# Kernel tuning notes

Hardware: AMD Instinct MI355X
Metric: run time of the kernel (lower is better)

Reference implementation:

```python
import jax, jax.numpy as jnp
import numpy as np

N_HEAD, D_HEAD, D_MODEL = 16, 64, 1024
BSZ, QLEN, MEMLEN = 4, 1024, 1024
KLEN = QLEN + MEMLEN
LN_EPS = 1e-5


def _rel_shift(x):
    # x: [b, q, k, n] -> Transformer-XL relative shift
    b, q, k, n = x.shape
    x = jnp.pad(x, ((0, 0), (0, 0), (1, 0), (0, 0)))  # [b, q, k+1, n]
    x = x.reshape(b, k + 1, q, n)[:, 1:]
    return x.reshape(b, q, k, n)


def _layer_norm(x, gamma, beta):
    mu = jnp.mean(x, axis=-1, keepdims=True)
    var = jnp.var(x, axis=-1, keepdims=True)
    return (x - mu) * jax.lax.rsqrt(var + LN_EPS) * gamma + beta


def setup_inputs() -> dict:
    key = jax.random.key(0)
    ks = jax.random.split(key, 8)
    w = jax.random.normal(ks[0], (BSZ, QLEN, D_MODEL), dtype=jnp.float32)
    r = jax.random.normal(ks[1], (1, KLEN, D_MODEL), dtype=jnp.float32)
    mem = jax.random.normal(ks[2], (BSZ, MEMLEN, D_MODEL), dtype=jnp.float32)
    # causal mask: key j visible iff j <= i + MEMLEN; 1 = masked
    i = jnp.arange(QLEN)[:, None]
    j = jnp.arange(KLEN)[None, :]
    attention_mask = (j > i + MEMLEN).astype(jnp.int32)
    s = 0.02
    qkv_w = jax.random.normal(ks[3], (3 * N_HEAD * D_HEAD, D_MODEL), dtype=jnp.float32) * s
    r_w = jax.random.normal(ks[4], (N_HEAD * D_HEAD, D_MODEL), dtype=jnp.float32) * s
    o_w = jax.random.normal(ks[5], (D_MODEL, N_HEAD * D_HEAD), dtype=jnp.float32) * s
    r_r_bias = jax.random.normal(ks[6], (N_HEAD, D_HEAD), dtype=jnp.float32) * s
    r_w_bias = jax.random.normal(ks[7], (N_HEAD, D_HEAD), dtype=jnp.float32) * s
    ln_gamma = jnp.ones((D_MODEL,), dtype=jnp.float32)
    ln_beta = jnp.zeros((D_MODEL,), dtype=jnp.float32)
    return {"w": w, "r": r, "mem": mem, "attention_mask": attention_mask,
            "qkv_w": qkv_w, "r_w": r_w, "o_w": o_w,
            "r_r_bias": r_r_bias, "r_w_bias": r_w_bias,
            "ln_gamma": ln_gamma, "ln_beta": ln_beta}


def reference(w, r, mem, attention_mask, qkv_w, r_w, o_w, r_r_bias, r_w_bias, ln_gamma, ln_beta):
    bsz, qlen, d_model = w.shape
    n_head, d_head = r_r_bias.shape
    scale = 1.0 / (d_head ** 0.5)
    cat = jnp.concatenate([mem, w], axis=1)                 # [b, klen, dm]
    heads = cat @ qkv_w.T                                   # post-lnorm: no pre-LN
    q, k, v = jnp.split(heads, 3, axis=-1)
    q = q[:, -qlen:]
    klen = k.shape[1]
    q = q.reshape(bsz, qlen, n_head, d_head)
    k = k.reshape(bsz, klen, n_head, d_head)
    v = v.reshape(bsz, klen, n_head, d_head)
    rk = (r @ r_w.T).reshape(-1, n_head, d_head)            # [rlen, n, d]
    AC = jnp.einsum('bind,bjnd->bijn', q + r_w_bias, k)
    BD = _rel_shift(jnp.einsum('bind,jnd->bijn', q + r_r_bias, rk))
    score = (AC + BD) * scale                               # [b, q, k, n]
    mask = (attention_mask == 1)[None, :, :, None]
    score = jnp.where(mask, -1e30, score)
    prob = jax.nn.softmax(score, axis=2)                    # softmax over keys
    vec = jnp.einsum('bijn,bjnd->bind', prob, v).reshape(bsz, qlen, n_head * d_head)
    attn_out = vec @ o_w.T
    # post layer-norm, deepnorm_alpha defaults to 1.0, dropout is identity (eval)
    return _layer_norm(w + attn_out, ln_gamma, ln_beta)
```

## Files before the change

kernel.cpp:

```cpp
#include <hip/hip_runtime.h>

typedef __attribute__((ext_vector_type(8))) __bf16 bf16x8;
typedef __attribute__((ext_vector_type(4))) __bf16 bf16x4;
typedef __attribute__((ext_vector_type(4))) float f32x4;

__device__ __forceinline__ f32x4 mfma16(bf16x8 a, bf16x8 b, f32x4 c) {
  return __builtin_amdgcn_mfma_f32_16x16x32_bf16(a, b, c, 0, 0, 0);
}

__device__ __forceinline__ void gload_lds16(const void* g, void* l) {
  __builtin_amdgcn_global_load_lds(
      (__attribute__((address_space(1))) void*)(void*)g,
      (__attribute__((address_space(3))) void*)l, 16, 0, 0);
}

__device__ __forceinline__ bf16x8 ldsfrag(const __bf16* base, int row, int lc) {
  return *(const bf16x8*)(base + row * 64 + ((lc ^ (row & 7)) << 3));
}


__global__ __launch_bounds__(256) void cast_plain(const float* __restrict__ in,
                                                  __bf16* __restrict__ out) {
  size_t t = (size_t)blockIdx.x * 256 + threadIdx.x;
  const float4* p = (const float4*)(in + t * 8);
  float4 a = p[0], b = p[1];
  bf16x8 v;
  v[0] = (__bf16)a.x; v[1] = (__bf16)a.y; v[2] = (__bf16)a.z; v[3] = (__bf16)a.w;
  v[4] = (__bf16)b.x; v[5] = (__bf16)b.y; v[6] = (__bf16)b.z; v[7] = (__bf16)b.w;
  *(bf16x8*)(out + t * 8) = v;
}

__global__ __launch_bounds__(256) void cast_cat(const float* __restrict__ mem,
                                                const float* __restrict__ w,
                                                __bf16* __restrict__ out) {
  size_t t = (size_t)blockIdx.x * 256 + threadIdx.x;
  size_t o = t * 8;
  int c = (int)(o & 1023);
  int row = (int)(o >> 10);
  int tt = row & 2047;
  int b = row >> 11;
  const float* src = (tt < 1024)
      ? (mem + ((size_t)(b * 1024 + tt) * 1024 + c))
      : (w + ((size_t)(b * 1024 + (tt - 1024)) * 1024 + c));
  float4 a = ((const float4*)src)[0], d = ((const float4*)src)[1];
  bf16x8 v;
  v[0] = (__bf16)a.x; v[1] = (__bf16)a.y; v[2] = (__bf16)a.z; v[3] = (__bf16)a.w;
  v[4] = (__bf16)d.x; v[5] = (__bf16)d.y; v[6] = (__bf16)d.z; v[7] = (__bf16)d.w;
  *(bf16x8*)(out + o) = v;
}

template <int MODE>
__global__ __launch_bounds__(256, 2) void gemm_bt(const __bf16* __restrict__ A,
                                                  const __bf16* __restrict__ B,
                                                  __bf16* __restrict__ Cb,
                                                  float* __restrict__ Cf,
                                                  const float* __restrict__ Res,
                                                  int M, int N, int K) {
  __shared__ __bf16 As[128 * 32];
  __shared__ __bf16 Bs[128 * 32];
  const int tid = threadIdx.x;
  const int wid = tid >> 6, lane = tid & 63;
  const int l15 = lane & 15, lhi = lane >> 4;
  const int wr = wid >> 1, wc = wid & 1;
  const size_t arow0 = (size_t)blockIdx.y * 128;
  const size_t brow0 = (size_t)blockIdx.x * 128;

  f32x4 acc[4][4] = {};

  const int c0 = tid, c1 = tid + 256;
  const int r0 = c0 >> 2, o0 = (c0 & 3) * 8;
  const int r1 = c1 >> 2, o1 = (c1 & 3) * 8;
  const __bf16* ga0 = A + (arow0 + r0) * K + o0;
  const __bf16* ga1 = A + (arow0 + r1) * K + o1;
  const __bf16* gb0 = B + (brow0 + r0) * K + o0;
  const __bf16* gb1 = B + (brow0 + r1) * K + o1;
  __bf16* la0 = As + wid * 512;
  __bf16* la1 = As + 2048 + wid * 512;
  __bf16* lb0 = Bs + wid * 512;
  __bf16* lb1 = Bs + 2048 + wid * 512;

  for (int k0 = 0; k0 < K; k0 += 32) {
    gload_lds16(ga0 + k0, la0);
    gload_lds16(ga1 + k0, la1);
    gload_lds16(gb0 + k0, lb0);
    gload_lds16(gb1 + k0, lb1);
    __syncthreads();
    bf16x8 af[4], bf[4];
#pragma unroll
    for (int m = 0; m < 4; ++m)
      af[m] = *(const bf16x8*)(As + (wr * 64 + m * 16 + l15) * 32 + lhi * 8);
#pragma unroll
    for (int n = 0; n < 4; ++n)
      bf[n] = *(const bf16x8*)(Bs + (wc * 64 + n * 16 + l15) * 32 + lhi * 8);
#pragma unroll
    for (int m = 0; m < 4; ++m)
#pragma unroll
      for (int n = 0; n < 4; ++n)
        acc[m][n] = mfma16(af[m], bf[n], acc[m][n]);
    __syncthreads();
  }

#pragma unroll
  for (int m = 0; m < 4; ++m)
#pragma unroll
    for (int n = 0; n < 4; ++n) {
      size_t row = arow0 + wr * 64 + m * 16 + lhi * 4;
      size_t col = brow0 + wc * 64 + n * 16 + l15;
#pragma unroll
      for (int j = 0; j < 4; ++j) {
        size_t idx = (row + j) * (size_t)N + col;
        float v = acc[m][n][j];
        if (MODE == 0) Cb[idx] = (__bf16)v;
        else Cf[idx] = v + Res[idx];
      }
    }
}

__global__ __launch_bounds__(256) void vtrans_kernel(const __bf16* __restrict__ heads,
                                                     __bf16* __restrict__ vT) {
  __shared__ __bf16 T[64][66];
  const int j0 = blockIdx.x * 64;
  const int h = blockIdx.y, b = blockIdx.z;
  const int tid = threadIdx.x;
  {
    int jj = tid >> 2, dq = tid & 3;
    const __bf16* src = heads + ((size_t)(b * 2048 + j0 + jj)) * 3072 + 2048 + h * 64 + dq * 16;
    bf16x8 a = *(const bf16x8*)src;
    bf16x8 c = *(const bf16x8*)(src + 8);
#pragma unroll
    for (int e = 0; e < 8; ++e) { T[jj][dq * 16 + e] = a[e]; T[jj][dq * 16 + 8 + e] = c[e]; }
  }
  __syncthreads();
  {
    int d = tid >> 2, jq = tid & 3;
    bf16x8 o0, o1;
#pragma unroll
    for (int e = 0; e < 8; ++e) { o0[e] = T[jq * 16 + e][d]; o1[e] = T[jq * 16 + 8 + e][d]; }
    __bf16* dst = vT + ((size_t)((b * 16 + h) * 64 + d)) * 2048 + j0 + jq * 16;
    *(bf16x8*)dst = o0;
    *(bf16x8*)(dst + 8) = o1;
  }
}

__global__ __launch_bounds__(256) void ackb_kernel(const __bf16* __restrict__ heads,
                                                   const float* __restrict__ r_w_bias,
                                                   float* __restrict__ ackb) {
  int gid = blockIdx.x * 256 + threadIdx.x;
  int j = gid & 2047, bh = gid >> 11, b = bh >> 4, h = bh & 15;
  const __bf16* kp = heads + ((size_t)(b * 2048 + j)) * 3072 + 1024 + h * 64;
  const float* bw = r_w_bias + h * 64;
  float s = 0.f;
#pragma unroll
  for (int o = 0; o < 8; ++o) {
    bf16x8 kv = *(const bf16x8*)(kp + o * 8);
#pragma unroll
    for (int e = 0; e < 8; ++e) s += (float)kv[e] * bw[o * 8 + e];
  }
  ackb[(size_t)bh * 2048 + j] = s * 0.125f;
}

__global__ __launch_bounds__(256) void brk_kernel(const __bf16* __restrict__ rk,
                                                  const float* __restrict__ r_r_bias,
                                                  float* __restrict__ brk) {
  int gid = blockIdx.x * 256 + threadIdx.x;
  int t = gid % 2304, h = gid / 2304;
  float s = 0.f;
  if (t < 2048) {
    const __bf16* rp = rk + (size_t)t * 1024 + h * 64;
    const float* br = r_r_bias + h * 64;
#pragma unroll
    for (int o = 0; o < 8; ++o) {
      bf16x8 rv = *(const bf16x8*)(rp + o * 8);
#pragma unroll
      for (int e = 0; e < 8; ++e) s += (float)rv[e] * br[o * 8 + e];
    }
  }
  brk[(size_t)h * 2304 + t] = s * 0.125f;
}

__global__ __launch_bounds__(256, 3) void attn_kernel(
    const __bf16* __restrict__ heads, const __bf16* __restrict__ rk,
    const __bf16* __restrict__ vT, const float* __restrict__ ackb,
    const float* __restrict__ brk, __bf16* __restrict__ vec) {
  __shared__ __bf16 Ks[64 * 64];
  __shared__ __bf16 Vt[64 * 64];
  __shared__ __bf16 Ring[128 * 64];
  __shared__ __bf16 BPa[4][16 * 88];

  const int lin = blockIdx.x;
  const int seq = lin >> 3;
  const int bq = 15 - (seq >> 3);
  const int rem = seq & 7;
  const int b = rem >> 1;
  const int h = (lin & 7) + ((rem & 1) << 3);
  const int base = bq << 6;

  const int tid = threadIdx.x;
  const int wid = tid >> 6, lane = tid & 63;
  const int l15 = lane & 15, lhi = lane >> 4;
  const int i0 = base + wid * 16;

  const int srow8 = lane >> 3;
  const int sch = (lane & 7) ^ (srow8 & 7);

  bf16x8 q0, q1;
  {
    const __bf16* qp =
        heads + ((size_t)(b * 2048 + 1024 + i0 + l15)) * 3072 + h * 64 + lhi * 8;
    bf16x8 a = *(const bf16x8*)qp;
    bf16x8 c = *(const bf16x8*)(qp + 32);
#pragma unroll
    for (int e = 0; e < 8; ++e) {
      q0[e] = (__bf16)((float)a[e] * 0.125f);
      q1[e] = (__bf16)((float)c[e] * 0.125f);
    }
  }

  const float* ackbp = ackb + ((size_t)(b * 16 + h)) * 2048;
  const float* brkp = brk + (size_t)h * 2304;
  __bf16* BP = BPa[wid];

  float m_run = -1e30f, l_run = 0.f;
  f32x4 accv[4] = {};

  {
    int r0 = 960 - base + wid * 16 + srow8;
    gload_lds16(rk + (size_t)r0 * 1024 + h * 64 + sch * 8,
                Ring + (((960 - base) + wid * 16) & 127) * 64);
    gload_lds16(rk + (size_t)(r0 + 8) * 1024 + h * 64 + sch * 8,
                Ring + (((960 - base) + wid * 16 + 8) & 127) * 64);
  }

  const int jmaxb = min(2048, base + 1088);
  for (int j0 = 0; j0 < jmaxb; j0 += 64) {
    __syncthreads();
    {
      const __bf16* kst =
          heads + ((size_t)(b * 2048 + j0 + wid * 16 + srow8)) * 3072 + 1024 + h * 64 + sch * 8;
      gload_lds16(kst, Ks + wid * 16 * 64);
      gload_lds16(kst + (size_t)8 * 3072, Ks + (wid * 16 + 8) * 64);
      const __bf16* vst =
          vT + ((size_t)((b * 16 + h) * 64 + wid * 16 + srow8)) * 2048 + j0 + sch * 8;
      gload_lds16(vst, Vt + wid * 16 * 64);
      gload_lds16(vst + (size_t)8 * 2048, Vt + (wid * 16 + 8) * 64);
      int T0 = j0 + 1024 - base;
      int rr = T0 + wid * 16 + srow8;
      gload_lds16(rk + (size_t)min(rr, 2047) * 1024 + h * 64 + sch * 8,
                  Ring + ((T0 + wid * 16) & 127) * 64);
      gload_lds16(rk + (size_t)min(rr + 8, 2047) * 1024 + h * 64 + sch * 8,
                  Ring + ((T0 + wid * 16 + 8) & 127) * 64);
    }
    __syncthreads();
    if (j0 >= i0 + 1040) continue;

    const int tbase = j0 + 1008 - i0;

#pragma unroll
    for (int ct = 0; ct < 5; ++ct) {
      int slot = (tbase + ct * 16 + l15) & 127;
      bf16x8 a0 = ldsfrag(Ring, slot, lhi);
      bf16x8 a1 = ldsfrag(Ring, slot, 4 + lhi);
      f32x4 init = *(const f32x4*)(brkp + tbase + ct * 16 + lhi * 4);
      f32x4 bd = mfma16(a1, q1, mfma16(a0, q0, init));
      bf16x4 bv;
      bv[0] = (__bf16)bd[0]; bv[1] = (__bf16)bd[1];
      bv[2] = (__bf16)bd[2]; bv[3] = (__bf16)bd[3];
      *(bf16x4*)(BP + l15 * 88 + ct * 16 + lhi * 4) = bv;
    }

    f32x4 st[4];
#pragma unroll
    for (int jt = 0; jt < 4; ++jt) {
      bf16x8 k0 = ldsfrag(Ks, jt * 16 + l15, lhi);
      bf16x8 k1 = ldsfrag(Ks, jt * 16 + l15, 4 + lhi);
      f32x4 init = *(const f32x4*)(ackbp + j0 + jt * 16 + lhi * 4);
      st[jt] = mfma16(k1, q1, mfma16(k0, q0, init));
    }

    float sv[4][4];
#pragma unroll
    for (int jt = 0; jt < 4; ++jt)
#pragma unroll
      for (int r2 = 0; r2 < 4; ++r2) {
        int jl = jt * 16 + lhi * 4 + r2;
        float v = st[jt][r2] + (float)BP[l15 * 88 + jl + 15 - l15];
        bool msk = (j0 + jl) > (i0 + l15 + 1024);
        sv[jt][r2] = msk ? -1e30f : v;
      }

    float mx = sv[0][0];
#pragma unroll
    for (int jt = 0; jt < 4; ++jt)
#pragma unroll
      for (int r2 = 0; r2 < 4; ++r2) mx = fmaxf(mx, sv[jt][r2]);
    mx = fmaxf(mx, __shfl_xor(mx, 16, 64));
    mx = fmaxf(mx, __shfl_xor(mx, 32, 64));
    float mn = fmaxf(m_run, mx);
    float corr = __expf(m_run - mn);
    float rs = 0.f;
#pragma unroll
    for (int jt = 0; jt < 4; ++jt)
#pragma unroll
      for (int r2 = 0; r2 < 4; ++r2) {
        float p = __expf(sv[jt][r2] - mn);
        sv[jt][r2] = p;
        rs += p;
      }
    rs += __shfl_xor(rs, 16, 64);
    rs += __shfl_xor(rs, 32, 64);
    m_run = mn;
    l_run = l_run * corr + rs;

    float c4[4];
#pragma unroll
    for (int r2 = 0; r2 < 4; ++r2) c4[r2] = __shfl(corr, lhi * 4 + r2, 64);
#pragma unroll
    for (int dt = 0; dt < 4; ++dt)
#pragma unroll
      for (int r2 = 0; r2 < 4; ++r2) accv[dt][r2] *= c4[r2];

#pragma unroll
    for (int jt = 0; jt < 4; ++jt) {
      bf16x4 pv;
      pv[0] = (__bf16)sv[jt][0]; pv[1] = (__bf16)sv[jt][1];
      pv[2] = (__bf16)sv[jt][2]; pv[3] = (__bf16)sv[jt][3];
      *(bf16x4*)(BP + l15 * 88 + jt * 16 + lhi * 4) = pv;
    }
    bf16x8 ap0 = *(const bf16x8*)(BP + l15 * 88 + lhi * 8);
    bf16x8 ap1 = *(const bf16x8*)(BP + l15 * 88 + 32 + lhi * 8);
#pragma unroll
    for (int dt = 0; dt < 4; ++dt) {
      bf16x8 vf0 = ldsfrag(Vt, dt * 16 + l15, lhi);
      bf16x8 vf1 = ldsfrag(Vt, dt * 16 + l15, 4 + lhi);
      accv[dt] = mfma16(ap1, vf1, mfma16(ap0, vf0, accv[dt]));
    }
  }

  float inv4[4];
#pragma unroll
  for (int r2 = 0; r2 < 4; ++r2) inv4[r2] = 1.0f / __shfl(l_run, lhi * 4 + r2, 64);
#pragma unroll
  for (int dt = 0; dt < 4; ++dt)
#pragma unroll
    for (int r2 = 0; r2 < 4; ++r2) {
      int i = i0 + lhi * 4 + r2;
      float v = accv[dt][r2] * inv4[r2];
      vec[((size_t)(b * 1024 + i)) * 1024 + h * 64 + dt * 16 + l15] = (__bf16)v;
    }
}

__global__ __launch_bounds__(256) void ln_kernel(const float* __restrict__ pre,
                                                 const float* __restrict__ gamma,
                                                 const float* __restrict__ beta,
                                                 float* __restrict__ out) {
  const int row = blockIdx.x;
  const int tid = threadIdx.x;
  const float4 v = ((const float4*)(pre + (size_t)row * 1024))[tid];
  float s = v.x + v.y + v.z + v.w;
  float s2 = v.x * v.x + v.y * v.y + v.z * v.z + v.w * v.w;
#pragma unroll
  for (int off = 1; off < 64; off <<= 1) {
    s += __shfl_xor(s, off, 64);
    s2 += __shfl_xor(s2, off, 64);
  }
  __shared__ float red[8];
  const int wid = tid >> 6;
  if ((tid & 63) == 0) { red[wid * 2] = s; red[wid * 2 + 1] = s2; }
  __syncthreads();
  s = red[0] + red[2] + red[4] + red[6];
  s2 = red[1] + red[3] + red[5] + red[7];
  float mu = s * (1.0f / 1024.0f);
  float var = s2 * (1.0f / 1024.0f) - mu * mu;
  float rstd = rsqrtf(var + 1e-5f);
  float4 g = ((const float4*)gamma)[tid];
  float4 be = ((const float4*)beta)[tid];
  float4 o;
  o.x = (v.x - mu) * rstd * g.x + be.x;
  o.y = (v.y - mu) * rstd * g.y + be.y;
  o.z = (v.z - mu) * rstd * g.z + be.z;
  o.w = (v.w - mu) * rstd * g.w + be.w;
  ((float4*)(out + (size_t)row * 1024))[tid] = o;
}

extern "C" void kernel_launch(void* const* d_in, const int* in_sizes, int n_in,
                              void* d_out, int out_size, void* d_ws, size_t ws_size,
                              hipStream_t stream) {
  const float* w = (const float*)d_in[0];
  const float* r = (const float*)d_in[1];
  const float* mem = (const float*)d_in[2];
  const float* qkv_w = (const float*)d_in[4];
  const float* r_w = (const float*)d_in[5];
  const float* o_w = (const float*)d_in[6];
  const float* r_r_bias = (const float*)d_in[7];
  const float* r_w_bias = (const float*)d_in[8];
  const float* gamma = (const float*)d_in[9];
  const float* beta = (const float*)d_in[10];
  float* out = (float*)d_out;

  char* ws = (char*)d_ws;
  const size_t MB = 1024 * 1024;
  __bf16* catB = (__bf16*)(ws + 0);
  __bf16* vT = (__bf16*)(ws + 0);
  float* pre = (float*)(ws + 0);
  __bf16* qkvwB = (__bf16*)(ws + 16 * MB);
  __bf16* rB = (__bf16*)(ws + 22 * MB);
  __bf16* rwB = (__bf16*)(ws + 26 * MB);
  __bf16* owB = (__bf16*)(ws + 28 * MB);
  __bf16* headsB = (__bf16*)(ws + 30 * MB);
  __bf16* rkB = (__bf16*)(ws + 78 * MB);
  __bf16* vecB = (__bf16*)(ws + 82 * MB);
  float* ackbF = (float*)(ws + 90 * MB);
  float* brkF = (float*)(ws + 91 * MB);

  cast_cat<<<4096, 256, 0, stream>>>(mem, w, catB);
  cast_plain<<<1536, 256, 0, stream>>>(qkv_w, qkvwB);
  cast_plain<<<1024, 256, 0, stream>>>(r, rB);
  cast_plain<<<512, 256, 0, stream>>>(r_w, rwB);
  cast_plain<<<512, 256, 0, stream>>>(o_w, owB);

  gemm_bt<0><<<dim3(24, 64), 256, 0, stream>>>(catB, qkvwB, headsB, nullptr, nullptr,
                                               8192, 3072, 1024);
  gemm_bt<0><<<dim3(8, 16), 256, 0, stream>>>(rB, rwB, rkB, nullptr, nullptr,
                                              2048, 1024, 1024);

  vtrans_kernel<<<dim3(32, 16, 4), 256, 0, stream>>>(headsB, vT);
  ackb_kernel<<<512, 256, 0, stream>>>(headsB, r_w_bias, ackbF);
  brk_kernel<<<144, 256, 0, stream>>>(rkB, r_r_bias, brkF);

  attn_kernel<<<1024, 256, 0, stream>>>(headsB, rkB, vT, ackbF, brkF, vecB);

  gemm_bt<1><<<dim3(8, 32), 256, 0, stream>>>(vecB, owB, nullptr, pre, w,
                                              4096, 1024, 1024);
  ln_kernel<<<4096, 256, 0, stream>>>(pre, gamma, beta, out);
}
```

Measured before the change: 298.3 us.

## Double-buffer attention K/V, register-prefetch rk, lazy rescale, skip unused Q GEMM tiles

The attention kernel now double-buffers the K and V tiles in LDS and drops the second barrier per iteration. The rk fragments are prefetched straight into registers in place of the LDS ring buffer. Softmax switches to exp2 with log2e folded into the scale, masking is confined to diagonal tiles, and the running-max rescale of the accumulator only happens when the max grows by more than a threshold. The QKV GEMM also skips the tiles that compute Q for memory rows, which are never used. The changes trade more LDS per block (and the dropped occupancy hint) for less waiting on loads and barriers. The lazy rescale lets values exceed 1 before normalisation, which can reduce accuracy.

```diff
diff --git a/kernel.cpp b/kernel.cpp
--- a/kernel.cpp
+++ b/kernel.cpp
@@ -3,6 +3,8 @@
 typedef __attribute__((ext_vector_type(8))) __bf16 bf16x8;
 typedef __attribute__((ext_vector_type(4))) __bf16 bf16x4;
 typedef __attribute__((ext_vector_type(4))) float f32x4;
+
+#define SCALE_LOG2E 0.18033688011112042f
 
 __device__ __forceinline__ f32x4 mfma16(bf16x8 a, bf16x8 b, f32x4 c) {
   return __builtin_amdgcn_mfma_f32_16x16x32_bf16(a, b, c, 0, 0, 0);
@@ -55,7 +57,8 @@
                                                   __bf16* __restrict__ Cb,
                                                   float* __restrict__ Cf,
                                                   const float* __restrict__ Res,
-                                                  int M, int N, int K) {
+                                                  int M, int N, int K, int skipq) {
+  if (skipq && blockIdx.x < 8 && (blockIdx.y & 15) < 8) return;
   __shared__ __bf16 As[128 * 32];
   __shared__ __bf16 Bs[128 * 32];
   const int tid = threadIdx.x;
@@ -156,7 +159,7 @@
 #pragma unroll
     for (int e = 0; e < 8; ++e) s += (float)kv[e] * bw[o * 8 + e];
   }
-  ackb[(size_t)bh * 2048 + j] = s * 0.125f;
+  ackb[(size_t)bh * 2048 + j] = s * SCALE_LOG2E;
 }
 
 __global__ __launch_bounds__(256) void brk_kernel(const __bf16* __restrict__ rk,
@@ -175,17 +178,16 @@
       for (int e = 0; e < 8; ++e) s += (float)rv[e] * br[o * 8 + e];
     }
   }
-  brk[(size_t)h * 2304 + t] = s * 0.125f;
-}
-
-__global__ __launch_bounds__(256, 3) void attn_kernel(
+  brk[(size_t)h * 2304 + t] = s * SCALE_LOG2E;
+}
+
+__global__ __launch_bounds__(256) void attn_kernel(
     const __bf16* __restrict__ heads, const __bf16* __restrict__ rk,
     const __bf16* __restrict__ vT, const float* __restrict__ ackb,
     const float* __restrict__ brk, __bf16* __restrict__ vec) {
-  __shared__ __bf16 Ks[64 * 64];
-  __shared__ __bf16 Vt[64 * 64];
-  __shared__ __bf16 Ring[128 * 64];
-  __shared__ __bf16 BPa[4][16 * 88];
+  __shared__ __bf16 Ks[2 * 4096];
+  __shared__ __bf16 Vt[2 * 4096];
+  __shared__ __bf16 Pool[4][2112];
 
   const int lin = blockIdx.x;
   const int seq = lin >> 3;
@@ -211,68 +213,79 @@
     bf16x8 c = *(const bf16x8*)(qp + 32);
 #pragma unroll
     for (int e = 0; e < 8; ++e) {
-      q0[e] = (__bf16)((float)a[e] * 0.125f);
-      q1[e] = (__bf16)((float)c[e] * 0.125f);
+      q0[e] = (__bf16)((float)a[e] * SCALE_LOG2E);
+      q1[e] = (__bf16)((float)c[e] * SCALE_LOG2E);
     }
   }
 
   const float* ackbp = ackb + ((size_t)(b * 16 + h)) * 2048;
   const float* brkp = brk + (size_t)h * 2304;
-  __bf16* BP = BPa[wid];
+  __bf16* BPW = Pool[wid];
 
   float m_run = -1e30f, l_run = 0.f;
   f32x4 accv[4] = {};
 
+#define STAGE_KV(J0, BUF)                                                              \
+  do {                                                                                 \
+    const __bf16* kst = heads +                                                        \
+        ((size_t)(b * 2048 + (J0) + wid * 16 + srow8)) * 3072 + 1024 + h * 64 + sch * 8; \
+    gload_lds16(kst, Ks + (BUF) * 4096 + wid * 16 * 64);                               \
+    gload_lds16(kst + (size_t)8 * 3072, Ks + (BUF) * 4096 + (wid * 16 + 8) * 64);      \
+    const __bf16* vst = vT +                                                           \
+        ((size_t)((b * 16 + h) * 64 + wid * 16 + srow8)) * 2048 + (J0) + sch * 8;      \
+    gload_lds16(vst, Vt + (BUF) * 4096 + wid * 16 * 64);                               \
+    gload_lds16(vst + (size_t)8 * 2048, Vt + (BUF) * 4096 + (wid * 16 + 8) * 64);      \
+  } while (0)
+
+  bf16x8 rka[5][2];
+  STAGE_KV(0, 0);
   {
-    int r0 = 960 - base + wid * 16 + srow8;
-    gload_lds16(rk + (size_t)r0 * 1024 + h * 64 + sch * 8,
-                Ring + (((960 - base) + wid * 16) & 127) * 64);
-    gload_lds16(rk + (size_t)(r0 + 8) * 1024 + h * 64 + sch * 8,
-                Ring + (((960 - base) + wid * 16 + 8) & 127) * 64);
+    const int tb0 = 1008 - i0;
+#pragma unroll
+    for (int ct = 0; ct < 5; ++ct) {
+      int t = min(tb0 + ct * 16 + l15, 2047);
+      const __bf16* rp = rk + (size_t)t * 1024 + h * 64 + lhi * 8;
+      rka[ct][0] = *(const bf16x8*)rp;
+      rka[ct][1] = *(const bf16x8*)(rp + 32);
+    }
   }
 
   const int jmaxb = min(2048, base + 1088);
   for (int j0 = 0; j0 < jmaxb; j0 += 64) {
+    const int buf = (j0 >> 6) & 1;
     __syncthreads();
-    {
-      const __bf16* kst =
-          heads + ((size_t)(b * 2048 + j0 + wid * 16 + srow8)) * 3072 + 1024 + h * 64 + sch * 8;
-      gload_lds16(kst, Ks + wid * 16 * 64);
-      gload_lds16(kst + (size_t)8 * 3072, Ks + (wid * 16 + 8) * 64);
-      const __bf16* vst =
-          vT + ((size_t)((b * 16 + h) * 64 + wid * 16 + srow8)) * 2048 + j0 + sch * 8;
-      gload_lds16(vst, Vt + wid * 16 * 64);
-      gload_lds16(vst + (size_t)8 * 2048, Vt + (wid * 16 + 8) * 64);
-      int T0 = j0 + 1024 - base;
-      int rr = T0 + wid * 16 + srow8;
-      gload_lds16(rk + (size_t)min(rr, 2047) * 1024 + h * 64 + sch * 8,
-                  Ring + ((T0 + wid * 16) & 127) * 64);
-      gload_lds16(rk + (size_t)min(rr + 8, 2047) * 1024 + h * 64 + sch * 8,
-                  Ring + ((T0 + wid * 16 + 8) & 127) * 64);
-    }
-    __syncthreads();
+    if (j0 + 64 < jmaxb) STAGE_KV(j0 + 64, buf ^ 1);
     if (j0 >= i0 + 1040) continue;
 
+    const __bf16* KsC = Ks + buf * 4096;
+    const __bf16* VtC = Vt + buf * 4096;
     const int tbase = j0 + 1008 - i0;
 
 #pragma unroll
     for (int ct = 0; ct < 5; ++ct) {
-      int slot = (tbase + ct * 16 + l15) & 127;
-      bf16x8 a0 = ldsfrag(Ring, slot, lhi);
-      bf16x8 a1 = ldsfrag(Ring, slot, 4 + lhi);
-      f32x4 init = *(const f32x4*)(brkp + tbase + ct * 16 + lhi * 4);
-      f32x4 bd = mfma16(a1, q1, mfma16(a0, q0, init));
+      int cb = ct * 16 + lhi * 4;
+      f32x4 init = *(const f32x4*)(brkp + tbase + cb);
+      f32x4 bd = mfma16(rka[ct][1], q1, mfma16(rka[ct][0], q0, init));
       bf16x4 bv;
       bv[0] = (__bf16)bd[0]; bv[1] = (__bf16)bd[1];
       bv[2] = (__bf16)bd[2]; bv[3] = (__bf16)bd[3];
-      *(bf16x4*)(BP + l15 * 88 + ct * 16 + lhi * 4) = bv;
+      *(bf16x4*)(BPW + l15 * 132 + cb) = bv;
+    }
+    rka[0][0] = rka[4][0];
+    rka[0][1] = rka[4][1];
+#pragma unroll
+    for (int ct = 1; ct < 5; ++ct) {
+      int t = min(tbase + 64 + ct * 16 + l15, 2047);
+      const __bf16* rp = rk + (size_t)t * 1024 + h * 64 + lhi * 8;
+      rka[ct][0] = *(const bf16x8*)rp;
+      rka[ct][1] = *(const bf16x8*)(rp + 32);
     }
 
     f32x4 st[4];
 #pragma unroll
     for (int jt = 0; jt < 4; ++jt) {
-      bf16x8 k0 = ldsfrag(Ks, jt * 16 + l15, lhi);
-      bf16x8 k1 = ldsfrag(Ks, jt * 16 + l15, 4 + lhi);
+      bf16x8 k0 = ldsfrag(KsC, jt * 16 + l15, lhi);
+      bf16x8 k1 = ldsfrag(KsC, jt * 16 + l15, 4 + lhi);
       f32x4 init = *(const f32x4*)(ackbp + j0 + jt * 16 + lhi * 4);
       st[jt] = mfma16(k1, q1, mfma16(k0, q0, init));
     }
@@ -283,10 +296,17 @@
 #pragma unroll
       for (int r2 = 0; r2 < 4; ++r2) {
         int jl = jt * 16 + lhi * 4 + r2;
-        float v = st[jt][r2] + (float)BP[l15 * 88 + jl + 15 - l15];
-        bool msk = (j0 + jl) > (i0 + l15 + 1024);
-        sv[jt][r2] = msk ? -1e30f : v;
+        sv[jt][r2] = st[jt][r2] + (float)BPW[l15 * 132 + jl + 15 - l15];
       }
+    if (j0 + 63 > i0 + 1024) {
+#pragma unroll
+      for (int jt = 0; jt < 4; ++jt)
+#pragma unroll
+        for (int r2 = 0; r2 < 4; ++r2) {
+          int jl = jt * 16 + lhi * 4 + r2;
+          if (j0 + jl > i0 + l15 + 1024) sv[jt][r2] = -1e30f;
+        }
+    }
 
     float mx = sv[0][0];
 #pragma unroll
@@ -295,46 +315,51 @@
       for (int r2 = 0; r2 < 4; ++r2) mx = fmaxf(mx, sv[jt][r2]);
     mx = fmaxf(mx, __shfl_xor(mx, 16, 64));
     mx = fmaxf(mx, __shfl_xor(mx, 32, 64));
-    float mn = fmaxf(m_run, mx);
-    float corr = __expf(m_run - mn);
+    const bool resc = __any(mx > m_run + 8.0f);
+    const float mn = resc ? fmaxf(m_run, mx) : m_run;
     float rs = 0.f;
 #pragma unroll
     for (int jt = 0; jt < 4; ++jt)
 #pragma unroll
       for (int r2 = 0; r2 < 4; ++r2) {
-        float p = __expf(sv[jt][r2] - mn);
+        float p = exp2f(sv[jt][r2] - mn);
         sv[jt][r2] = p;
         rs += p;
       }
     rs += __shfl_xor(rs, 16, 64);
     rs += __shfl_xor(rs, 32, 64);
-    m_run = mn;
-    l_run = l_run * corr + rs;
-
-    float c4[4];
-#pragma unroll
-    for (int r2 = 0; r2 < 4; ++r2) c4[r2] = __shfl(corr, lhi * 4 + r2, 64);
-#pragma unroll
-    for (int dt = 0; dt < 4; ++dt)
-#pragma unroll
-      for (int r2 = 0; r2 < 4; ++r2) accv[dt][r2] *= c4[r2];
+    if (resc) {
+      float corr = exp2f(m_run - mn);
+      float c4[4];
+#pragma unroll
+      for (int r2 = 0; r2 < 4; ++r2) c4[r2] = __shfl(corr, lhi * 4 + r2, 64);
+#pragma unroll
+      for (int dt = 0; dt < 4; ++dt)
+#pragma unroll
+        for (int r2 = 0; r2 < 4; ++r2) accv[dt][r2] *= c4[r2];
+      m_run = mn;
+      l_run = l_run * corr + rs;
+    } else {
+      l_run += rs;
+    }
 
 #pragma unroll
     for (int jt = 0; jt < 4; ++jt) {
       bf16x4 pv;
       pv[0] = (__bf16)sv[jt][0]; pv[1] = (__bf16)sv[jt][1];
       pv[2] = (__bf16)sv[jt][2]; pv[3] = (__bf16)sv[jt][3];
-      *(bf16x4*)(BP + l15 * 88 + jt * 16 + lhi * 4) = pv;
-    }
-    bf16x8 ap0 = *(const bf16x8*)(BP + l15 * 88 + lhi * 8);
-    bf16x8 ap1 = *(const bf16x8*)(BP + l15 * 88 + 32 + lhi * 8);
+      *(bf16x4*)(BPW + l15 * 72 + jt * 16 + lhi * 4) = pv;
+    }
+    bf16x8 ap0 = *(const bf16x8*)(BPW + l15 * 72 + lhi * 8);
+    bf16x8 ap1 = *(const bf16x8*)(BPW + l15 * 72 + 32 + lhi * 8);
 #pragma unroll
     for (int dt = 0; dt < 4; ++dt) {
-      bf16x8 vf0 = ldsfrag(Vt, dt * 16 + l15, lhi);
-      bf16x8 vf1 = ldsfrag(Vt, dt * 16 + l15, 4 + lhi);
+      bf16x8 vf0 = ldsfrag(VtC, dt * 16 + l15, lhi);
+      bf16x8 vf1 = ldsfrag(VtC, dt * 16 + l15, 4 + lhi);
       accv[dt] = mfma16(ap1, vf1, mfma16(ap0, vf0, accv[dt]));
     }
   }
+#undef STAGE_KV
 
   float inv4[4];
 #pragma unroll
@@ -419,9 +444,9 @@
   cast_plain<<<512, 256, 0, stream>>>(o_w, owB);
 
   gemm_bt<0><<<dim3(24, 64), 256, 0, stream>>>(catB, qkvwB, headsB, nullptr, nullptr,
-                                               8192, 3072, 1024);
+                                               8192, 3072, 1024, 1);
   gemm_bt<0><<<dim3(8, 16), 256, 0, stream>>>(rB, rwB, rkB, nullptr, nullptr,
-                                              2048, 1024, 1024);
+                                              2048, 1024, 1024, 0);
 
   vtrans_kernel<<<dim3(32, 16, 4), 256, 0, stream>>>(headsB, vT);
   ackb_kernel<<<512, 256, 0, stream>>>(headsB, r_w_bias, ackbF);
@@ -430,6 +455,6 @@
   attn_kernel<<<1024, 256, 0, stream>>>(headsB, rkB, vT, ackbF, brkF, vecB);
 
   gemm_bt<1><<<dim3(8, 32), 256, 0, stream>>>(vecB, owB, nullptr, pre, w,
-                                              4096, 1024, 1024);
+                                              4096, 1024, 1024, 0);
   ln_kernel<<<4096, 256, 0, stream>>>(pre, gamma, beta, out);
 }
```

After: 354.4 us. +18.8%, slower.
